# Optimization experiments

Measured on AMD Instinct MI355X. Metric: run time of the kernel, lower is better.

## Reference

```python
import jax, jax.numpy as jnp
import numpy as np

N = 23
B = 16384
T = 12


def setup_inputs() -> dict:
    key = jax.random.key(0)
    k1, k2, k3 = jax.random.split(key, 3)
    flow_x = jax.random.normal(k1, (B, N, N, T), dtype=jnp.float32)
    adj = jax.random.randint(k2, (N, N), 0, 2).astype(jnp.int32)
    W = jax.random.uniform(k3, (N, N, N), dtype=jnp.float32)
    return {"flow_x": flow_x, "adj": adj, "W": W}


def reference(flow_x, adj, W):
    # data = flow_x[:, :, :, -1]  -> (B, N, N), last time step
    data = flow_x[..., -1]
    # force self-loops: adj[i][i] = 1
    adj = adj.at[jnp.diag_indices(N)].set(1)
    # shift each row of W so its minimum is >= 0 (only if min < 0)
    mn = jnp.min(W, axis=-1, keepdims=True)          # (N, N, 1)
    mn = jnp.minimum(mn, 0.0)                         # where(min>0, 0, min)
    attention = W - mn                                # (N, N, N)
    # zero out attention[:, i, j] wherever adj[i, j] == 0 (mask over dims 1,2)
    mask = (adj != 0).astype(attention.dtype)         # (N, N)
    attention = attention * mask[None, :, :]
    # row-normalize over last dim
    attention = attention / jnp.sum(attention, axis=-1, keepdims=True)
    # original: x[b, i, :] = attention[i] @ data[b, :, i]
    # x[b, i, k] = sum_m attention[i, k, m] * data[b, m, i]
    x = jnp.einsum('ikm,bmi->bik', attention, data)   # (B, N, N)
    return x[..., None]                               # (B, N, N, 1)
```

## Files before the change

kernel.cpp:

```cpp
#include <hip/hip_runtime.h>

#define N 23
#define NN (N * N)
#define TT 12
#define BPB 8
#define THREADS 256

__global__ void attn_kernel(const int* __restrict__ adj,
                            const float* __restrict__ W,
                            float* __restrict__ att) {
    int idx = blockIdx.x * blockDim.x + threadIdx.x;
    if (idx >= NN) return;
    int k = idx % N;
    const float* row = W + idx * N;
    float mn = 0.f;
#pragma unroll
    for (int m = 0; m < N; ++m) mn = fminf(mn, row[m]);
    float v[N];
    float s = 0.f;
#pragma unroll
    for (int m = 0; m < N; ++m) {
        int a = (m == k) ? 1 : adj[k * N + m];
        float x = (a != 0) ? (row[m] - mn) : 0.f;
        v[m] = x;
        s += x;
    }
    float inv = 1.f / s;
#pragma unroll
    for (int m = 0; m < N; ++m) att[idx * N + m] = v[m] * inv;
}

__global__ __launch_bounds__(THREADS) void gat_kernel(const float* __restrict__ flow,
                                                      const float* __restrict__ att_g,
                                                      float* __restrict__ out) {
    __shared__ float att[NN * N];
    for (int t = threadIdx.x; t < NN * N; t += THREADS) att[t] = att_g[t];
    __syncthreads();

    const int bbase = blockIdx.x * BPB;
#pragma unroll 1
    for (int o = threadIdx.x; o < BPB * NN; o += THREADS) {
        int bofs = o / NN;
        int r = o - bofs * NN;
        int i = r / N;
        int b = bbase + bofs;
        const float* dptr = flow + ((size_t)b * NN + i) * TT + (TT - 1);
        const float* arow = att + r * N;
        float acc = 0.f;
#pragma unroll
        for (int m = 0; m < N; ++m)
            acc = fmaf(arow[m], dptr[(size_t)m * (N * TT)], acc);
        out[(size_t)b * NN + r] = acc;
    }
}

extern "C" void kernel_launch(void* const* d_in, const int* in_sizes, int n_in,
                              void* d_out, int out_size, void* d_ws, size_t ws_size,
                              hipStream_t stream) {
    const float* flow = (const float*)d_in[0];
    const int* adj = (const int*)d_in[1];
    const float* W = (const float*)d_in[2];
    float* out = (float*)d_out;
    float* att = (float*)d_ws;

    const int B = in_sizes[0] / (NN * TT);

    attn_kernel<<<(NN + THREADS - 1) / THREADS, THREADS, 0, stream>>>(adj, W, att);
    gat_kernel<<<B / BPB, THREADS, 0, stream>>>(flow, att, out);
}
```

Baseline: 568.1 us.

## Stage last-timestep data in LDS and read padded attention from global

```diff
diff --git a/kernel.cpp b/kernel.cpp
--- a/kernel.cpp
+++ b/kernel.cpp
@@ -1,10 +1,15 @@
 #include <hip/hip_runtime.h>
 
 #define N 23
-#define NN (N * N)
+#define NN 529
 #define TT 12
 #define BPB 8
 #define THREADS 256
+#define ATT_LD 24
+#define DATA_LD 24
+#define DATA_BSTRIDE (N * DATA_LD)
+
+typedef float f4 __attribute__((ext_vector_type(4)));
 
 __global__ void attn_kernel(const int* __restrict__ adj,
                             const float* __restrict__ W,
@@ -27,30 +32,64 @@
     }
     float inv = 1.f / s;
 #pragma unroll
-    for (int m = 0; m < N; ++m) att[idx * N + m] = v[m] * inv;
+    for (int m = 0; m < N; ++m) att[idx * ATT_LD + m] = v[m] * inv;
+    att[idx * ATT_LD + N] = 0.f;
 }
 
 __global__ __launch_bounds__(THREADS) void gat_kernel(const float* __restrict__ flow,
-                                                      const float* __restrict__ att_g,
+                                                      const float* __restrict__ att,
                                                       float* __restrict__ out) {
-    __shared__ float att[NN * N];
-    for (int t = threadIdx.x; t < NN * N; t += THREADS) att[t] = att_g[t];
+    __shared__ float data[BPB * DATA_BSTRIDE];
+    const int bbase = blockIdx.x * BPB;
+
+    for (int idx = threadIdx.x; idx < BPB * NN; idx += THREADS) {
+        int bl = idx / NN;
+        int r = idx - bl * NN;
+        int m = r / N;
+        int i = r - m * N;
+        const f4* src = (const f4*)(flow + (size_t)(bbase + bl) * (NN * TT))
+                        + (m * (N * TT / 4) + i * 3 + 2);
+        f4 v = __builtin_nontemporal_load(src);
+        data[bl * DATA_BSTRIDE + i * DATA_LD + m] = v.w;
+    }
     __syncthreads();
 
-    const int bbase = blockIdx.x * BPB;
-#pragma unroll 1
     for (int o = threadIdx.x; o < BPB * NN; o += THREADS) {
-        int bofs = o / NN;
-        int r = o - bofs * NN;
+        int bl = o / NN;
+        int r = o - bl * NN;
         int i = r / N;
-        int b = bbase + bofs;
-        const float* dptr = flow + ((size_t)b * NN + i) * TT + (TT - 1);
-        const float* arow = att + r * N;
-        float acc = 0.f;
-#pragma unroll
-        for (int m = 0; m < N; ++m)
-            acc = fmaf(arow[m], dptr[(size_t)m * (N * TT)], acc);
-        out[(size_t)b * NN + r] = acc;
+
+        const f4* arow = (const f4*)(att + r * ATT_LD);
+        const f4* drow = (const f4*)(data + bl * DATA_BSTRIDE + i * DATA_LD);
+
+        f4 a0 = arow[0], a1 = arow[1], a2 = arow[2], a3 = arow[3], a4 = arow[4], a5 = arow[5];
+        f4 d0 = drow[0], d1 = drow[1], d2 = drow[2], d3 = drow[3], d4 = drow[4], d5 = drow[5];
+
+        float acc = a0.x * d0.x;
+        acc = fmaf(a0.y, d0.y, acc);
+        acc = fmaf(a0.z, d0.z, acc);
+        acc = fmaf(a0.w, d0.w, acc);
+        acc = fmaf(a1.x, d1.x, acc);
+        acc = fmaf(a1.y, d1.y, acc);
+        acc = fmaf(a1.z, d1.z, acc);
+        acc = fmaf(a1.w, d1.w, acc);
+        acc = fmaf(a2.x, d2.x, acc);
+        acc = fmaf(a2.y, d2.y, acc);
+        acc = fmaf(a2.z, d2.z, acc);
+        acc = fmaf(a2.w, d2.w, acc);
+        acc = fmaf(a3.x, d3.x, acc);
+        acc = fmaf(a3.y, d3.y, acc);
+        acc = fmaf(a3.z, d3.z, acc);
+        acc = fmaf(a3.w, d3.w, acc);
+        acc = fmaf(a4.x, d4.x, acc);
+        acc = fmaf(a4.y, d4.y, acc);
+        acc = fmaf(a4.z, d4.z, acc);
+        acc = fmaf(a4.w, d4.w, acc);
+        acc = fmaf(a5.x, d5.x, acc);
+        acc = fmaf(a5.y, d5.y, acc);
+        acc = fmaf(a5.z, d5.z, acc);
+
+        out[(size_t)(bbase + bl) * NN + r] = acc;
     }
 }
 
```

After: 546.1 us. 1.04x faster.

## Fuse attention normalization into GAT kernel and stage last-step data in LDS

Applied to the files above, without the earlier changes.

```diff
diff --git a/kernel.cpp b/kernel.cpp
--- a/kernel.cpp
+++ b/kernel.cpp
@@ -1,56 +1,117 @@
 #include <hip/hip_runtime.h>
 
 #define N 23
-#define NN (N * N)
+#define NN 529
 #define TT 12
 #define BPB 8
 #define THREADS 256
+#define DATA_LD 24
+#define DATA_BSTRIDE (N * DATA_LD)
+#define STG ((BPB * NN + THREADS - 1) / THREADS)
 
-__global__ void attn_kernel(const int* __restrict__ adj,
-                            const float* __restrict__ W,
-                            float* __restrict__ att) {
-    int idx = blockIdx.x * blockDim.x + threadIdx.x;
-    if (idx >= NN) return;
-    int k = idx % N;
-    const float* row = W + idx * N;
+typedef float f4 __attribute__((ext_vector_type(4)));
+
+__device__ __forceinline__ void compute_arow(int r, const int* __restrict__ adj,
+                                             const float* __restrict__ W, float* a) {
+    int i = r / N;
+    int k = r - i * N;
+    const float* wrow = W + r * N;
     float mn = 0.f;
 #pragma unroll
-    for (int m = 0; m < N; ++m) mn = fminf(mn, row[m]);
-    float v[N];
+    for (int m = 0; m < N; ++m) { a[m] = wrow[m]; mn = fminf(mn, a[m]); }
     float s = 0.f;
 #pragma unroll
     for (int m = 0; m < N; ++m) {
-        int a = (m == k) ? 1 : adj[k * N + m];
-        float x = (a != 0) ? (row[m] - mn) : 0.f;
-        v[m] = x;
+        int msk = (m == k) ? 1 : adj[k * N + m];
+        float x = (msk != 0) ? (a[m] - mn) : 0.f;
+        a[m] = x;
         s += x;
     }
     float inv = 1.f / s;
 #pragma unroll
-    for (int m = 0; m < N; ++m) att[idx * N + m] = v[m] * inv;
+    for (int m = 0; m < N; ++m) a[m] *= inv;
 }
 
-__global__ __launch_bounds__(THREADS) void gat_kernel(const float* __restrict__ flow,
-                                                      const float* __restrict__ att_g,
-                                                      float* __restrict__ out) {
-    __shared__ float att[NN * N];
-    for (int t = threadIdx.x; t < NN * N; t += THREADS) att[t] = att_g[t];
+__device__ __forceinline__ void emit_row(int r, const float* a, const float* data,
+                                         float* __restrict__ out, int bbase) {
+    int i = r / N;
+    const float* drow0 = data + i * DATA_LD;
+#pragma unroll
+    for (int bl = 0; bl < BPB; ++bl) {
+        const f4* d = (const f4*)(drow0 + bl * DATA_BSTRIDE);
+        f4 d0 = d[0], d1 = d[1], d2 = d[2], d3 = d[3], d4 = d[4], d5 = d[5];
+        float acc = a[0] * d0.x;
+        acc = fmaf(a[1],  d0.y, acc);
+        acc = fmaf(a[2],  d0.z, acc);
+        acc = fmaf(a[3],  d0.w, acc);
+        acc = fmaf(a[4],  d1.x, acc);
+        acc = fmaf(a[5],  d1.y, acc);
+        acc = fmaf(a[6],  d1.z, acc);
+        acc = fmaf(a[7],  d1.w, acc);
+        acc = fmaf(a[8],  d2.x, acc);
+        acc = fmaf(a[9],  d2.y, acc);
+        acc = fmaf(a[10], d2.z, acc);
+        acc = fmaf(a[11], d2.w, acc);
+        acc = fmaf(a[12], d3.x, acc);
+        acc = fmaf(a[13], d3.y, acc);
+        acc = fmaf(a[14], d3.z, acc);
+        acc = fmaf(a[15], d3.w, acc);
+        acc = fmaf(a[16], d4.x, acc);
+        acc = fmaf(a[17], d4.y, acc);
+        acc = fmaf(a[18], d4.z, acc);
+        acc = fmaf(a[19], d4.w, acc);
+        acc = fmaf(a[20], d5.x, acc);
+        acc = fmaf(a[21], d5.y, acc);
+        acc = fmaf(a[22], d5.z, acc);
+        __builtin_nontemporal_store(acc, out + (size_t)(bbase + bl) * NN + r);
+    }
+}
+
+__global__ __launch_bounds__(THREADS) void fused_gat(const float* __restrict__ flow,
+                                                     const int* __restrict__ adj,
+                                                     const float* __restrict__ W,
+                                                     float* __restrict__ out) {
+    __shared__ float data[BPB * DATA_BSTRIDE];
+    const int tid = threadIdx.x;
+    const int bbase = blockIdx.x * BPB;
+
+    float sv[STG];
+    int laddr[STG];
+#pragma unroll
+    for (int it = 0; it < STG; ++it) {
+        int idx = tid + it * THREADS;
+        bool ok = (idx < BPB * NN);
+        int idc = ok ? idx : 0;
+        int bl = idc / NN;
+        int r = idc - bl * NN;
+        int m = r / N;
+        int i = r - m * N;
+        const f4* src = (const f4*)(flow + (size_t)(bbase + bl) * (NN * TT))
+                        + (m * (N * TT / 4) + i * 3 + 2);
+        f4 v = __builtin_nontemporal_load(src);
+        sv[it] = v.w;
+        laddr[it] = ok ? (bl * DATA_BSTRIDE + i * DATA_LD + m) : -1;
+    }
+
+    float a0[N];
+    compute_arow(tid, adj, W, a0);
+
+#pragma unroll
+    for (int it = 0; it < STG; ++it)
+        if (laddr[it] >= 0) data[laddr[it]] = sv[it];
     __syncthreads();
 
-    const int bbase = blockIdx.x * BPB;
-#pragma unroll 1
-    for (int o = threadIdx.x; o < BPB * NN; o += THREADS) {
-        int bofs = o / NN;
-        int r = o - bofs * NN;
-        int i = r / N;
-        int b = bbase + bofs;
-        const float* dptr = flow + ((size_t)b * NN + i) * TT + (TT - 1);
-        const float* arow = att + r * N;
-        float acc = 0.f;
-#pragma unroll
-        for (int m = 0; m < N; ++m)
-            acc = fmaf(arow[m], dptr[(size_t)m * (N * TT)], acc);
-        out[(size_t)b * NN + r] = acc;
+    emit_row(tid, a0, data, out, bbase);
+
+    {
+        float a1[N];
+        compute_arow(tid + THREADS, adj, W, a1);
+        emit_row(tid + THREADS, a1, data, out, bbase);
+    }
+    if (tid < NN - 2 * THREADS) {
+        float a2[N];
+        compute_arow(tid + 2 * THREADS, adj, W, a2);
+        emit_row(tid + 2 * THREADS, a2, data, out, bbase);
     }
 }
 
@@ -61,10 +122,8 @@
     const int* adj = (const int*)d_in[1];
     const float* W = (const float*)d_in[2];
     float* out = (float*)d_out;
-    float* att = (float*)d_ws;
 
     const int B = in_sizes[0] / (NN * TT);
 
-    attn_kernel<<<(NN + THREADS - 1) / THREADS, THREADS, 0, stream>>>(adj, W, att);
-    gat_kernel<<<B / BPB, THREADS, 0, stream>>>(flow, att, out);
+    fused_gat<<<B / BPB, THREADS, 0, stream>>>(flow, adj, W, out);
 }
```

Measured after the change: 541.5 us. -4.7%, faster.
